# Optimization experiments

Hardware: AMD Instinct MI355X
Metric: run time of the kernel (lower is better)

## Reference

```python
import jax, jax.numpy as jnp
import numpy as np

N, E, IN_DIM, HID, MAXW, HEADS = 20000, 640000, 128, 256, 512, 32
BN_EPS = 1e-5


def setup_inputs() -> dict:
    key = jax.random.key(0)
    ks = jax.random.split(key, 10)
    x = jax.random.normal(ks[0], (N, IN_DIM), dtype=jnp.float32)
    edge_index = jax.random.randint(ks[1], (2, E), 0, N, dtype=jnp.int64)
    s = 0.02
    # backbone GIN layer: Linear(in_dim -> hidden) applied to (x + sum of neighbors)
    Wb = jax.random.normal(ks[2], (IN_DIM, HID), dtype=jnp.float32) * s
    bb = jnp.zeros((HID,), dtype=jnp.float32)
    # per-head hourglass: Linear(HID->MAXW) + BN + ReLU, then Linear(MAXW->HID)
    W1 = jax.random.normal(ks[3], (HEADS, HID, MAXW), dtype=jnp.float32) * s
    b1 = jnp.zeros((HEADS, MAXW), dtype=jnp.float32)
    gamma = jnp.ones((HEADS, MAXW), dtype=jnp.float32)
    beta = jnp.zeros((HEADS, MAXW), dtype=jnp.float32)
    W2 = jax.random.normal(ks[4], (HEADS, MAXW, HID), dtype=jnp.float32) * s
    b2 = jnp.zeros((HEADS, HID), dtype=jnp.float32)
    return {"x": x, "edge_index": edge_index, "Wb": Wb, "bb": bb,
            "W1": W1, "b1": b1, "gamma": gamma, "beta": beta,
            "W2": W2, "b2": b2}


def reference(x, edge_index, Wb, bb, W1, b1, gamma, beta, W2, b2):
    src, dst = edge_index[0], edge_index[1]
    # GIN-style aggregation (eps=0): self + sum of neighbor features
    agg = x + jax.ops.segment_sum(x[src], dst, num_segments=x.shape[0])
    h = jax.nn.relu(agg @ Wb + bb)                          # [N, HID]
    # all 32 heads as one batched GEMM
    z = jnp.einsum('nd,hdm->hnm', h, W1) + b1[:, None, :]   # [H, N, MAXW]
    # per-head BatchNorm1d in training mode: batch stats over nodes, biased var
    mean = jnp.mean(z, axis=1, keepdims=True)
    var = jnp.var(z, axis=1, keepdims=True)
    zn = (z - mean) * jax.lax.rsqrt(var + BN_EPS)
    a = jax.nn.relu(zn * gamma[:, None, :] + beta[:, None, :])
    # final per-head projection, stacked to [N, H, HID]
    out = jnp.einsum('hnm,hmd->nhd', a, W2) + b2[None, :, :]
    return out
```

## Files before the change

kernel.cpp:

```cpp
#include <hip/hip_runtime.h>
#include <stdint.h>

#define N_NODES 20000
#define E_EDGES 640000
#define IN_DIM  128
#define HID     256
#define MAXW    512
#define HEADS   32
#define BN_EPS  1e-5f
#define NT      20480
#define NB_SCAN 79

typedef __attribute__((ext_vector_type(8))) short bf16x8;
typedef __attribute__((ext_vector_type(4))) float f32x4;
typedef __attribute__((ext_vector_type(16))) float f32x16;
typedef unsigned short ushort_t;

static __device__ __forceinline__ float bf2f(ushort_t u){
  union { unsigned int i; float f; } v; v.i = ((unsigned int)u) << 16; return v.f;
}
static __device__ __forceinline__ ushort_t f2bf(float f){
  union { float f; unsigned int i; } v; v.f = f;
  unsigned int r = v.i + 0x7fffu + ((v.i >> 16) & 1u);
  return (ushort_t)(r >> 16);
}

__global__ void k_initdet(const int* __restrict__ ei, float* __restrict__ G,
                          float* __restrict__ s, int* __restrict__ deg,
                          int* __restrict__ flag, ushort_t* __restrict__ hT){
  int i = blockIdx.x * blockDim.x + threadIdx.x;
  int stride = gridDim.x * blockDim.x;
  float4 z4 = make_float4(0.f, 0.f, 0.f, 0.f);
  float4* Gd = (float4*)G;
  for (int j = i; j < 256 * 256 / 4; j += stride) Gd[j] = z4;
  for (int j = i; j < N_NODES; j += stride) deg[j] = 0;
  if (i < 256) s[i] = 0.f;
  uint4 zi = make_uint4(0u, 0u, 0u, 0u);
  for (int j = i; j < 256 * 60; j += stride){
    int c = j / 60, o = (j % 60) * 8;
    *(uint4*)(hT + (size_t)c * NT + N_NODES + o) = zi;
  }
  if (blockIdx.x == 0){
    __shared__ int any_nz;
    if (threadIdx.x == 0) any_nz = 0;
    __syncthreads();
    int nz = 0;
    for (int k = threadIdx.x; k < 4096; k += blockDim.x)
      if (ei[2 * k + 1] != 0) nz = 1;
    if (nz) atomicOr(&any_nz, 1);
    __syncthreads();
    if (threadIdx.x == 0) flag[0] = (any_nz == 0) ? 1 : 0;
  }
}

__global__ __launch_bounds__(256) void k_hist(const int* __restrict__ ei,
                                              const int* __restrict__ flag,
                                              int* __restrict__ deg){
  int e = blockIdx.x * 256 + threadIdx.x;
  if (e >= E_EDGES) return;
  int src, dst;
  if (flag[0]){ src = ei[2 * e]; dst = ei[2 * E_EDGES + 2 * e]; }
  else        { src = ei[e];     dst = ei[E_EDGES + e]; }
  if ((unsigned)src >= N_NODES || (unsigned)dst >= N_NODES) return;
  atomicAdd(&deg[dst], 1);
}

__global__ __launch_bounds__(256) void k_scan1(const int* __restrict__ deg,
                                               int* __restrict__ bsum){
  __shared__ int ws[4];
  int b = blockIdx.x, t = threadIdx.x, i = b * 256 + t;
  int v = (i < N_NODES) ? deg[i] : 0;
  #pragma unroll
  for (int o = 32; o; o >>= 1) v += __shfl_down(v, o);
  if ((t & 63) == 0) ws[t >> 6] = v;
  __syncthreads();
  if (t == 0) bsum[b] = ws[0] + ws[1] + ws[2] + ws[3];
}

__global__ __launch_bounds__(256) void k_scan3(const int* __restrict__ deg,
                                               const int* __restrict__ bsum,
                                               int* __restrict__ start,
                                               int* __restrict__ cursor){
  __shared__ int a[2][256];
  __shared__ int base;
  int b = blockIdx.x, t = threadIdx.x, i = b * 256 + t;
  if (t == 0){
    int r = 0;
    for (int k = 0; k < b; k++) r += bsum[k];
    base = r;
  }
  int v = (i < N_NODES) ? deg[i] : 0;
  a[0][t] = v;
  __syncthreads();
  int pb = 0;
  for (int o = 1; o < 256; o <<= 1){
    int x = a[pb][t] + ((t >= o) ? a[pb][t - o] : 0);
    a[pb ^ 1][t] = x;
    __syncthreads();
    pb ^= 1;
  }
  if (i < N_NODES){
    int ex = base + a[pb][t] - v;
    start[i] = ex; cursor[i] = ex;
  }
}

__global__ __launch_bounds__(256) void k_scatter(const int* __restrict__ ei,
                                                 const int* __restrict__ flag,
                                                 int* __restrict__ cursor,
                                                 int* __restrict__ eids){
  int e = blockIdx.x * 256 + threadIdx.x;
  if (e >= E_EDGES) return;
  int src, dst;
  if (flag[0]){ src = ei[2 * e]; dst = ei[2 * E_EDGES + 2 * e]; }
  else        { src = ei[e];     dst = ei[E_EDGES + e]; }
  if ((unsigned)src >= N_NODES || (unsigned)dst >= N_NODES) return;
  int p = atomicAdd(&cursor[dst], 1);
  eids[p] = src;
}

__global__ __launch_bounds__(256) void k_agg(const float* __restrict__ x,
                                             const int* __restrict__ start,
                                             const int* __restrict__ deg,
                                             const int* __restrict__ eids,
                                             float* __restrict__ agg){
  int wid = (blockIdx.x * 256 + threadIdx.x) >> 6;
  int lane = threadIdx.x & 63;
  if (wid >= N_NODES) return;
  int s0 = start[wid], d = deg[wid];
  float2 acc = *(const float2*)(x + (size_t)wid * IN_DIM + 2 * lane);
  int i = 0;
  for (; i + 4 <= d; i += 4){
    int e0 = eids[s0+i], e1 = eids[s0+i+1], e2 = eids[s0+i+2], e3 = eids[s0+i+3];
    float2 v0 = *(const float2*)(x + (size_t)e0 * IN_DIM + 2 * lane);
    float2 v1 = *(const float2*)(x + (size_t)e1 * IN_DIM + 2 * lane);
    float2 v2 = *(const float2*)(x + (size_t)e2 * IN_DIM + 2 * lane);
    float2 v3 = *(const float2*)(x + (size_t)e3 * IN_DIM + 2 * lane);
    acc.x += (v0.x + v1.x) + (v2.x + v3.x);
    acc.y += (v0.y + v1.y) + (v2.y + v3.y);
  }
  for (; i < d; i++){
    int e0 = eids[s0+i];
    float2 v0 = *(const float2*)(x + (size_t)e0 * IN_DIM + 2 * lane);
    acc.x += v0.x; acc.y += v0.y;
  }
  *(float2*)(agg + (size_t)wid * IN_DIM + 2 * lane) = acc;
}

__global__ __launch_bounds__(256) void k_backbone(const float* __restrict__ agg,
                                                  const float* __restrict__ Wb,
                                                  const float* __restrict__ bb,
                                                  ushort_t* __restrict__ hbf,
                                                  ushort_t* __restrict__ hT,
                                                  float* __restrict__ s){
  __shared__ float WbS[32][256];
  __shared__ float aggS[32][36];
  int c = threadIdx.x;
  int n0 = blockIdx.x * 32;
  float acc[32];
  float bias = bb[c];
  #pragma unroll
  for (int i = 0; i < 32; i++) acc[i] = bias;
  for (int dc = 0; dc < 4; ++dc){
    __syncthreads();
    const float4* wsrc = (const float4*)(Wb + dc * 32 * 256);
    float4* wdst = (float4*)&WbS[0][0];
    #pragma unroll
    for (int i = 0; i < 8; i++) wdst[c + i * 256] = wsrc[c + i * 256];
    {
      int n = c >> 3, c4 = (c & 7) * 4;
      float4 v = *(const float4*)(agg + (size_t)(n0 + n) * IN_DIM + dc * 32 + c4);
      aggS[n][c4 + 0] = v.x; aggS[n][c4 + 1] = v.y;
      aggS[n][c4 + 2] = v.z; aggS[n][c4 + 3] = v.w;
    }
    __syncthreads();
    for (int d = 0; d < 32; ++d){
      float w = WbS[d][c];
      #pragma unroll
      for (int n = 0; n < 32; n++) acc[n] += aggS[n][d] * w;
    }
  }
  float ls = 0.f;
  ushort_t hrow[32];
  #pragma unroll
  for (int n = 0; n < 32; n++){
    float hv = acc[n] > 0.f ? acc[n] : 0.f;
    ushort_t hb = f2bf(hv);
    hbf[(size_t)(n0 + n) * HID + c] = hb;
    hrow[n] = hb;
    ls += bf2f(hb);
  }
  #pragma unroll
  for (int i = 0; i < 4; i++)
    *(uint4*)(hT + (size_t)c * NT + n0 + i * 8) = *(uint4*)(hrow + i * 8);
  unsafeAtomicAdd(&s[c], ls);
}

__global__ __launch_bounds__(256) void k_gram2(const ushort_t* __restrict__ hT,
                                               float* __restrict__ G){
  const int t = threadIdx.x;
  const int w = t >> 6, l = t & 63;
  const int s = blockIdx.x, hh = blockIdx.y;
  const int wr = w >> 1, wc = w & 1;
  const int ca = hh * 128 + wr * 64;
  const int cb = wc * 128;
  const int l31 = l & 31, l5 = l >> 5;
  f32x16 acc[2][4];
  #pragma unroll
  for (int a = 0; a < 2; a++)
    #pragma unroll
    for (int b = 0; b < 4; b++)
      #pragma unroll
      for (int r = 0; r < 16; r++) acc[a][b][r] = 0.f;

  const size_t kb0 = (size_t)s * 512 + l5 * 8;
  for (int ks = 0; ks < 32; ks++){
    size_t k = kb0 + ks * 16;
    bf16x8 af[2], bfr[4];
    #pragma unroll
    for (int a = 0; a < 2; a++)
      af[a] = *(const bf16x8*)(hT + (size_t)(ca + a * 32 + l31) * NT + k);
    #pragma unroll
    for (int b = 0; b < 4; b++)
      bfr[b] = *(const bf16x8*)(hT + (size_t)(cb + b * 32 + l31) * NT + k);
    #pragma unroll
    for (int a = 0; a < 2; a++)
      #pragma unroll
      for (int b = 0; b < 4; b++)
        acc[a][b] = __builtin_amdgcn_mfma_f32_32x32x16_bf16(af[a], bfr[b], acc[a][b], 0, 0, 0);
  }
  #pragma unroll
  for (int a = 0; a < 2; a++)
    #pragma unroll
    for (int b = 0; b < 4; b++)
      #pragma unroll
      for (int r = 0; r < 16; r++){
        int grow = (r & 3) + 8 * (r >> 2) + 4 * l5;
        unsafeAtomicAdd(&G[(size_t)(ca + a * 32 + grow) * 256 + cb + b * 32 + l31], acc[a][b][r]);
      }
}

__global__ __launch_bounds__(256) void k_transpose(const float* __restrict__ W1,
                                                   const float* __restrict__ W2,
                                                   ushort_t* __restrict__ w1t,
                                                   ushort_t* __restrict__ w2t){
  __shared__ float tile[32][33];
  int which = blockIdx.z, h = blockIdx.y, b = blockIdx.x;
  const float* src; int R, C;
  if (which == 0){ src = W1 + (size_t)h * 256 * 512; R = 256; C = 512; }
  else           { src = W2 + (size_t)h * 512 * 256; R = 512; C = 256; }
  int tcn = C >> 5;
  int tr = b / tcn, tc = b % tcn;
  int r0 = tr * 32, c0 = tc * 32;
  int tx = threadIdx.x & 31, ty = threadIdx.x >> 5;
  #pragma unroll
  for (int i = 0; i < 32; i += 8) tile[ty + i][tx] = src[(size_t)(r0 + ty + i) * C + c0 + tx];
  __syncthreads();
  if (which == 0){
    ushort_t* dst = w1t + (size_t)h * 512 * 256;
    #pragma unroll
    for (int i = 0; i < 32; i += 8){
      int M = c0 + ty + i;
      int D = r0 + tx;
      int D2 = (((D >> 3) ^ (M & 7)) << 3) | (D & 7);
      dst[(size_t)M * 256 + D2] = f2bf(tile[tx][ty + i]);
    }
  } else {
    ushort_t* dst = w2t + (size_t)h * 256 * 512;
    #pragma unroll
    for (int i = 0; i < 32; i += 8){
      int dd = c0 + ty + i;
      int m  = r0 + tx;
      int g2 = ((m >> 3) & 3) ^ (dd & 3) ^ ((dd >> 2) & 3);
      size_t idx = (size_t)(m >> 5) * 8192 + dd * 32 + (g2 << 3) + (m & 7);
      dst[idx] = f2bf(tile[tx][ty + i]);
    }
  }
}

__global__ __launch_bounds__(256) void k_stats(const float* __restrict__ G,
                                               const float* __restrict__ s,
                                               const ushort_t* __restrict__ w1t,
                                               const float* __restrict__ b1,
                                               const float* __restrict__ gamma,
                                               const float* __restrict__ beta,
                                               float* __restrict__ As,
                                               float* __restrict__ Bs){
  __shared__ ushort_t wL[256][64];
  __shared__ float GL[16][256];
  __shared__ float sL[256];
  __shared__ float red[4][64];
  int h = blockIdx.y, m0 = blockIdx.x * 64;
  int t = threadIdx.x, m = t & 63, q = t >> 6;
  {
    int mm = t >> 2, part = t & 3;
    int Mrow = m0 + mm;
    const ushort_t* srcr = w1t + ((size_t)h * 512 + Mrow) * 256;
    #pragma unroll
    for (int k4 = 0; k4 < 16; ++k4){
      int kb = part * 64 + k4 * 4;
      int eo = (((kb >> 3) ^ (Mrow & 7)) << 3) | (kb & 7);
      ushort4 v = *(const ushort4*)(srcr + eo);
      wL[kb+0][mm]=v.x; wL[kb+1][mm]=v.y; wL[kb+2][mm]=v.z; wL[kb+3][mm]=v.w;
    }
  }
  sL[t & 255] = s[t & 255];
  float quad = 0.f;
  for (int dc = 0; dc < 16; ++dc){
    __syncthreads();
    const float4* gs = (const float4*)(G + (size_t)dc * 16 * 256);
    float4* gd = (float4*)&GL[0][0];
    #pragma unroll
    for (int i = 0; i < 4; i++) gd[t + i * 256] = gs[t + i * 256];
    __syncthreads();
    #pragma unroll
    for (int i = 0; i < 4; i++){
      int dl = q * 4 + i;
      float wd = bf2f(wL[dc * 16 + dl][m]);
      float u = 0.f;
      for (int k = 0; k < 256; ++k) u += GL[dl][k] * bf2f(wL[k][m]);
      quad += wd * u;
    }
  }
  red[q][m] = quad;
  __syncthreads();
  if (q == 0){
    float qd = red[0][m] + red[1][m] + red[2][m] + red[3][m];
    float dot_s = 0.f;
    for (int k = 0; k < 256; ++k) dot_s += sL[k] * bf2f(wL[k][m]);
    float b1v = b1[(size_t)h * 512 + m0 + m];
    float invN = 1.f / (float)N_NODES;
    float mean = dot_s * invN + b1v;
    float ez2 = (qd + 2.f * b1v * dot_s) * invN + b1v * b1v;
    float var = ez2 - mean * mean;
    float rstd = rsqrtf(var + BN_EPS);
    float gv = gamma[(size_t)h * 512 + m0 + m];
    float be = beta[(size_t)h * 512 + m0 + m];
    float Av = rstd * gv;
    As[(size_t)h * 512 + m0 + m] = Av;
    Bs[(size_t)h * 512 + m0 + m] = be - mean * Av;
  }
}

__global__ __launch_bounds__(512, 2) void k_main(const ushort_t* __restrict__ hbf,
                                                 const ushort_t* __restrict__ w1t,
                                                 const ushort_t* __restrict__ w2t,
                                                 const float* __restrict__ As,
                                                 const float* __restrict__ Bs,
                                                 const float* __restrict__ b2,
                                                 float* __restrict__ out){
  __shared__ __align__(16) char lds_all[86016];
  const int h = blockIdx.y;
  const int n0 = blockIdx.x * 256;
  const int t = threadIdx.x;
  const int w = t >> 6, l = t & 63;
  const int l15 = l & 15, l4 = l >> 4;
  const int nw = n0 + w * 32;
  const f32x4 fzero = {0.f, 0.f, 0.f, 0.f};
  const bf16x8 bzero = {0,0,0,0,0,0,0,0};
  char* asw = lds_all + 65536 + w * 2560;

  bf16x8 afr[2][8];
  #pragma unroll
  for (int nset = 0; nset < 2; nset++){
    int row = nw + nset * 16 + l15;
    const ushort_t* p = hbf + (size_t)row * HID + l4 * 8;
    #pragma unroll
    for (int kk = 0; kk < 8; kk++){
      bf16x8 v = bzero;
      if (row < N_NODES) v = *(const bf16x8*)(p + kk * 32);
      afr[nset][kk] = v;
    }
  }
  f32x4 oacc[16][2];
  #pragma unroll
  for (int i = 0; i < 16; i++){ oacc[i][0] = fzero; oacc[i][1] = fzero; }

  const float* Asp = As + (size_t)h * 512;
  const float* Bsp = Bs + (size_t)h * 512;
  const char* w1g = (const char*)(w1t + (size_t)h * 512 * 256);
  const char* w2g = (const char*)(w2t + (size_t)h * 256 * 512);
  const int woff = w * 2048 + l * 16;

  {
    __builtin_amdgcn_global_load_lds((const __attribute__((address_space(1))) void*)(w1g + woff),
                                     (__attribute__((address_space(3))) void*)(lds_all + w * 2048), 16, 0, 0);
    __builtin_amdgcn_global_load_lds((const __attribute__((address_space(1))) void*)(w1g + woff + 1024),
                                     (__attribute__((address_space(3))) void*)(lds_all + w * 2048 + 1024), 16, 0, 0);
    __builtin_amdgcn_global_load_lds((const __attribute__((address_space(1))) void*)(w2g + woff),
                                     (__attribute__((address_space(3))) void*)(lds_all + 16384 + w * 2048), 16, 0, 0);
    __builtin_amdgcn_global_load_lds((const __attribute__((address_space(1))) void*)(w2g + woff + 1024),
                                     (__attribute__((address_space(3))) void*)(lds_all + 16384 + w * 2048 + 1024), 16, 0, 0);
  }
  __syncthreads();

  const int win = (l4 & 1) * 32;
  const unsigned sel = (l4 >> 1) ? 0x07060302u : 0x05040100u;

  for (int c = 0; c < 16; ++c){
    const int cur = c & 1;
    const int mc0 = c * 32;
    const bool pf = (c < 15);
    if (pf){
      const int nb = (c + 1) * 16384;
      char* db = lds_all + (cur ^ 1) * 32768;
      __builtin_amdgcn_global_load_lds((const __attribute__((address_space(1))) void*)(w1g + nb + woff),
                                       (__attribute__((address_space(3))) void*)(db + w * 2048), 16, 0, 0);
      __builtin_amdgcn_global_load_lds((const __attribute__((address_space(1))) void*)(w1g + nb + woff + 1024),
                                       (__attribute__((address_space(3))) void*)(db + w * 2048 + 1024), 16, 0, 0);
      __builtin_amdgcn_global_load_lds((const __attribute__((address_space(1))) void*)(w2g + nb + woff),
                                       (__attribute__((address_space(3))) void*)(db + 16384 + w * 2048), 16, 0, 0);
      __builtin_amdgcn_global_load_lds((const __attribute__((address_space(1))) void*)(w2g + nb + woff + 1024),
                                       (__attribute__((address_space(3))) void*)(db + 16384 + w * 2048 + 1024), 16, 0, 0);
    }
    const char* w1b = lds_all + cur * 32768;
    const char* w2b = lds_all + cur * 32768 + 16384;

    f32x4 zt[2][2];
    zt[0][0] = fzero; zt[0][1] = fzero; zt[1][0] = fzero; zt[1][1] = fzero;
    __builtin_amdgcn_s_setprio(1);
    #pragma unroll
    for (int kk = 0; kk < 8; kk++){
      #pragma unroll
      for (int ct = 0; ct < 2; ct++){
        int r1 = ct * 16 + l15;
        int gr = kk * 4 + l4;
        bf16x8 wf = *(const bf16x8*)(w1b + r1 * 512 + ((gr ^ (r1 & 7)) * 16));
        zt[0][ct] = __builtin_amdgcn_mfma_f32_16x16x32_bf16(wf, afr[0][kk], zt[0][ct], 0, 0, 0);
        zt[1][ct] = __builtin_amdgcn_mfma_f32_16x16x32_bf16(wf, afr[1][kk], zt[1][ct], 0, 0, 0);
      }
    }
    __builtin_amdgcn_s_setprio(0);

    {
      float4 Av0 = *(const float4*)(Asp + mc0 + l4 * 4);
      float4 Bv0 = *(const float4*)(Bsp + mc0 + l4 * 4);
      float4 Av1 = *(const float4*)(Asp + mc0 + 16 + l4 * 4);
      float4 Bv1 = *(const float4*)(Bsp + mc0 + 16 + l4 * 4);
      #pragma unroll
      for (int nset = 0; nset < 2; nset++){
        float c00 = zt[nset][0][0] * Av0.x + Bv0.x; c00 = c00 > 0.f ? c00 : 0.f;
        float c01 = zt[nset][0][1] * Av0.y + Bv0.y; c01 = c01 > 0.f ? c01 : 0.f;
        float c02 = zt[nset][0][2] * Av0.z + Bv0.z; c02 = c02 > 0.f ? c02 : 0.f;
        float c03 = zt[nset][0][3] * Av0.w + Bv0.w; c03 = c03 > 0.f ? c03 : 0.f;
        float c10 = zt[nset][1][0] * Av1.x + Bv1.x; c10 = c10 > 0.f ? c10 : 0.f;
        float c11 = zt[nset][1][1] * Av1.y + Bv1.y; c11 = c11 > 0.f ? c11 : 0.f;
        float c12 = zt[nset][1][2] * Av1.z + Bv1.z; c12 = c12 > 0.f ? c12 : 0.f;
        float c13 = zt[nset][1][3] * Av1.w + Bv1.w; c13 = c13 > 0.f ? c13 : 0.f;
        uint4 pk;
        pk.x = (unsigned)f2bf(c00) | ((unsigned)f2bf(c10) << 16);
        pk.y = (unsigned)f2bf(c01) | ((unsigned)f2bf(c11) << 16);
        pk.z = (unsigned)f2bf(c02) | ((unsigned)f2bf(c12) << 16);
        pk.w = (unsigned)f2bf(c03) | ((unsigned)f2bf(c13) << 16);
        *(uint4*)(asw + (nset * 16 + l15) * 80 + l4 * 16) = pk;
      }
    }
    bf16x8 aa[2];
    #pragma unroll
    for (int nset = 0; nset < 2; nset++){
      const char* rp = asw + (nset * 16 + l15) * 80 + win;
      uint4 wa = *(const uint4*)(rp);
      uint4 wb = *(const uint4*)(rp + 16);
      unsigned o0 = __builtin_amdgcn_perm(wa.y, wa.x, sel);
      unsigned o1 = __builtin_amdgcn_perm(wa.w, wa.z, sel);
      unsigned o2 = __builtin_amdgcn_perm(wb.y, wb.x, sel);
      unsigned o3 = __builtin_amdgcn_perm(wb.w, wb.z, sel);
      uint4 q = make_uint4(o0, o1, o2, o3);
      aa[nset] = *(bf16x8*)&q;
    }

    __builtin_amdgcn_s_setprio(1);
    #pragma unroll
    for (int ddt = 0; ddt < 16; ddt++){
      int dd = ddt * 16 + l15;
      int g2 = l4 ^ (dd & 3) ^ ((dd >> 2) & 3);
      bf16x8 wf2 = *(const bf16x8*)(w2b + dd * 64 + g2 * 16);
      oacc[ddt][0] = __builtin_amdgcn_mfma_f32_16x16x32_bf16(wf2, aa[0], oacc[ddt][0], 0, 0, 0);
      oacc[ddt][1] = __builtin_amdgcn_mfma_f32_16x16x32_bf16(wf2, aa[1], oacc[ddt][1], 0, 0, 0);
    }
    __builtin_amdgcn_s_setprio(0);

    __syncthreads();
  }

  char* slice = lds_all + w * 8192;
  const int gsl = l & 31;
  const int rhalf = l >> 5;
  #pragma unroll
  for (int nset = 0; nset < 2; nset++){
    #pragma unroll
    for (int half = 0; half < 2; half++){
      #pragma unroll
      for (int dq = 0; dq < 8; dq++){
        int ddt = half * 8 + dq;
        *(f32x4*)(slice + l15 * 512 + (((dq * 4 + l4) ^ (l15 & 7)) * 16)) = oacc[ddt][nset];
      }
      float4 b2v = *(const float4*)(b2 + (size_t)h * 256 + half * 128 + gsl * 4);
      #pragma unroll
      for (int j = 0; j < 8; j++){
        int rr = rhalf + j * 2;
        f32x4 v = *(const f32x4*)(slice + rr * 512 + ((gsl ^ (rr & 7)) * 16));
        int n = nw + nset * 16 + rr;
        if (n < N_NODES){
          float4 o;
          o.x = v[0] + b2v.x; o.y = v[1] + b2v.y;
          o.z = v[2] + b2v.z; o.w = v[3] + b2v.w;
          *(float4*)(out + (size_t)n * (HEADS * HID) + h * HID + half * 128 + gsl * 4) = o;
        }
      }
    }
  }
}

extern "C" void kernel_launch(void* const* d_in, const int* in_sizes, int n_in,
                              void* d_out, int out_size, void* d_ws, size_t ws_size,
                              hipStream_t stream){
  const float* x     = (const float*)d_in[0];
  const int*   ei    = (const int*)  d_in[1];
  const float* Wb    = (const float*)d_in[2];
  const float* bb    = (const float*)d_in[3];
  const float* W1    = (const float*)d_in[4];
  const float* b1    = (const float*)d_in[5];
  const float* gamma = (const float*)d_in[6];
  const float* beta  = (const float*)d_in[7];
  const float* W2    = (const float*)d_in[8];
  const float* b2    = (const float*)d_in[9];
  float* out = (float*)d_out;

  char* ws = (char*)d_ws;
  size_t off = 0;
  auto alloc = [&](size_t bytes){ void* p = ws + off; off += (bytes + 255) & ~(size_t)255; return p; };
  float*    agg  = (float*)   alloc((size_t)N_NODES * IN_DIM * 4);
  ushort_t* hbf  = (ushort_t*)alloc((size_t)N_NODES * HID * 2);
  ushort_t* w1t  = (ushort_t*)alloc((size_t)HEADS * MAXW * HID * 2);
  ushort_t* w2t  = (ushort_t*)alloc((size_t)HEADS * HID * MAXW * 2);
  float*    G    = (float*)   alloc(256 * 256 * 4);
  float*    s    = (float*)   alloc(256 * 4);
  float*    As   = (float*)   alloc((size_t)HEADS * MAXW * 4);
  float*    Bs   = (float*)   alloc((size_t)HEADS * MAXW * 4);
  int*      flg  = (int*)     alloc(256);
  int*      deg  = (int*)     alloc((size_t)N_NODES * 4);
  int*      st   = (int*)     alloc((size_t)N_NODES * 4);
  int*      cur  = (int*)     alloc((size_t)N_NODES * 4);
  int*      eids = (int*)     alloc((size_t)E_EDGES * 4);
  ushort_t* hT   = (ushort_t*)alloc((size_t)HID * NT * 2);
  int*      bsum = (int*)     alloc(NB_SCAN * 4);

  hipLaunchKernelGGL(k_initdet,   dim3(512),         dim3(256), 0, stream, ei, G, s, deg, flg, hT);
  hipLaunchKernelGGL(k_hist,      dim3(2500),        dim3(256), 0, stream, ei, flg, deg);
  hipLaunchKernelGGL(k_scan1,     dim3(NB_SCAN),     dim3(256), 0, stream, deg, bsum);
  hipLaunchKernelGGL(k_scan3,     dim3(NB_SCAN),     dim3(256), 0, stream, deg, bsum, st, cur);
  hipLaunchKernelGGL(k_scatter,   dim3(2500),        dim3(256), 0, stream, ei, flg, cur, eids);
  hipLaunchKernelGGL(k_agg,       dim3(5000),        dim3(256), 0, stream, x, st, deg, eids, agg);
  hipLaunchKernelGGL(k_backbone,  dim3(625),         dim3(256), 0, stream, agg, Wb, bb, hbf, hT, s);
  hipLaunchKernelGGL(k_gram2,     dim3(40, 2),       dim3(256), 0, stream, hT, G);
  hipLaunchKernelGGL(k_transpose, dim3(128, 32, 2),  dim3(256), 0, stream, W1, W2, w1t, w2t);
  hipLaunchKernelGGL(k_stats,     dim3(8, 32),       dim3(256), 0, stream, G, s, w1t, b1, gamma, beta, As, Bs);
  hipLaunchKernelGGL(k_main,      dim3(79, 32),      dim3(512), 0, stream, hbf, w1t, w2t, As, Bs, b2, out);
}
```

Before: 805.7 us.

## Double chunk size per pipeline stage in main kernel and vectorize weight transpose stores

The main fused kernel now loads two 32-wide M chunks of W1/W2 per pipeline stage, with a 64KB double buffer, and processes them in an unrolled sub-loop. This halves the number of barriers and prefetch rounds. LDS use grows from about 84KB to about 148KB per block, which likely limits occupancy to one block per CU despite launch_bounds(512,2). The bf16 pack now uses the hardware v_cvt_pk_bf16_f32 instruction. The transpose kernel writes 16-byte vector stores from half the threads instead of scattered 2-byte stores.

```diff
diff --git a/kernel.cpp b/kernel.cpp
--- a/kernel.cpp
+++ b/kernel.cpp
@@ -23,6 +23,11 @@
   union { float f; unsigned int i; } v; v.f = f;
   unsigned int r = v.i + 0x7fffu + ((v.i >> 16) & 1u);
   return (ushort_t)(r >> 16);
+}
+static __device__ __forceinline__ unsigned cvtpk(float lo, float hi){
+  unsigned r;
+  asm("v_cvt_pk_bf16_f32 %0, %1, %2" : "=v"(r) : "v"(lo), "v"(hi));
+  return r;
 }
 
 __global__ void k_initdet(const int* __restrict__ ei, float* __restrict__ G,
@@ -256,25 +261,27 @@
   #pragma unroll
   for (int i = 0; i < 32; i += 8) tile[ty + i][tx] = src[(size_t)(r0 + ty + i) * C + c0 + tx];
   __syncthreads();
+  int tid = threadIdx.x;
+  if (tid >= 128) return;
   if (which == 0){
-    ushort_t* dst = w1t + (size_t)h * 512 * 256;
-    #pragma unroll
-    for (int i = 0; i < 32; i += 8){
-      int M = c0 + ty + i;
-      int D = r0 + tx;
-      int D2 = (((D >> 3) ^ (M & 7)) << 3) | (D & 7);
-      dst[(size_t)M * 256 + D2] = f2bf(tile[tx][ty + i]);
-    }
+    int mloc = tid & 31, dg = tid >> 5;
+    int M = c0 + mloc;
+    int Dg = (r0 >> 3) + dg;
+    ushort_t tmp[8];
+    #pragma unroll
+    for (int j = 0; j < 8; j++) tmp[j] = f2bf(tile[dg * 8 + j][mloc]);
+    ushort_t* dst = w1t + (size_t)h * 512 * 256 + (size_t)M * 256 + ((Dg ^ (M & 7)) << 3);
+    *(uint4*)dst = *(uint4*)tmp;
   } else {
-    ushort_t* dst = w2t + (size_t)h * 256 * 512;
-    #pragma unroll
-    for (int i = 0; i < 32; i += 8){
-      int dd = c0 + ty + i;
-      int m  = r0 + tx;
-      int g2 = ((m >> 3) & 3) ^ (dd & 3) ^ ((dd >> 2) & 3);
-      size_t idx = (size_t)(m >> 5) * 8192 + dd * 32 + (g2 << 3) + (m & 7);
-      dst[idx] = f2bf(tile[tx][ty + i]);
-    }
+    int ddloc = tid & 31, mo = tid >> 5;
+    int dd = c0 + ddloc;
+    int m0g = r0 + mo * 8;
+    int g2 = ((m0g >> 3) & 3) ^ (dd & 3) ^ ((dd >> 2) & 3);
+    ushort_t tmp[8];
+    #pragma unroll
+    for (int j = 0; j < 8; j++) tmp[j] = f2bf(tile[mo * 8 + j][ddloc]);
+    ushort_t* dst = w2t + (size_t)h * 256 * 512 + (size_t)(m0g >> 5) * 8192 + dd * 32 + (g2 << 3);
+    *(uint4*)dst = *(uint4*)tmp;
   }
 }
 
@@ -342,6 +349,10 @@
   }
 }
 
+#define GLDS(srcp, dstp) __builtin_amdgcn_global_load_lds( \
+    (const __attribute__((address_space(1))) void*)(srcp), \
+    (__attribute__((address_space(3))) void*)(dstp), 16, 0, 0)
+
 __global__ __launch_bounds__(512, 2) void k_main(const ushort_t* __restrict__ hbf,
                                                  const ushort_t* __restrict__ w1t,
                                                  const ushort_t* __restrict__ w2t,
@@ -349,7 +360,7 @@
                                                  const float* __restrict__ Bs,
                                                  const float* __restrict__ b2,
                                                  float* __restrict__ out){
-  __shared__ __align__(16) char lds_all[86016];
+  __shared__ __align__(16) char lds_all[151552];
   const int h = blockIdx.y;
   const int n0 = blockIdx.x * 256;
   const int t = threadIdx.x;
@@ -358,7 +369,7 @@
   const int nw = n0 + w * 32;
   const f32x4 fzero = {0.f, 0.f, 0.f, 0.f};
   const bf16x8 bzero = {0,0,0,0,0,0,0,0};
-  char* asw = lds_all + 65536 + w * 2560;
+  char* asw = lds_all + 131072 + w * 2560;
 
   bf16x8 afr[2][8];
   #pragma unroll
@@ -383,103 +394,106 @@
   const int woff = w * 2048 + l * 16;
 
   {
-    __builtin_amdgcn_global_load_lds((const __attribute__((address_space(1))) void*)(w1g + woff),
-                                     (__attribute__((address_space(3))) void*)(lds_all + w * 2048), 16, 0, 0);
-    __builtin_amdgcn_global_load_lds((const __attribute__((address_space(1))) void*)(w1g + woff + 1024),
-                                     (__attribute__((address_space(3))) void*)(lds_all + w * 2048 + 1024), 16, 0, 0);
-    __builtin_amdgcn_global_load_lds((const __attribute__((address_space(1))) void*)(w2g + woff),
-                                     (__attribute__((address_space(3))) void*)(lds_all + 16384 + w * 2048), 16, 0, 0);
-    __builtin_amdgcn_global_load_lds((const __attribute__((address_space(1))) void*)(w2g + woff + 1024),
-                                     (__attribute__((address_space(3))) void*)(lds_all + 16384 + w * 2048 + 1024), 16, 0, 0);
+    char* db = lds_all;
+    GLDS(w1g + woff,                 db + w * 2048);
+    GLDS(w1g + woff + 1024,          db + w * 2048 + 1024);
+    GLDS(w1g + 16384 + woff,         db + 16384 + w * 2048);
+    GLDS(w1g + 16384 + woff + 1024,  db + 16384 + w * 2048 + 1024);
+    GLDS(w2g + woff,                 db + 32768 + w * 2048);
+    GLDS(w2g + woff + 1024,          db + 32768 + w * 2048 + 1024);
+    GLDS(w2g + 16384 + woff,         db + 49152 + w * 2048);
+    GLDS(w2g + 16384 + woff + 1024,  db + 49152 + w * 2048 + 1024);
   }
   __syncthreads();
 
   const int win = (l4 & 1) * 32;
   const unsigned sel = (l4 >> 1) ? 0x07060302u : 0x05040100u;
 
-  for (int c = 0; c < 16; ++c){
-    const int cur = c & 1;
-    const int mc0 = c * 32;
-    const bool pf = (c < 15);
-    if (pf){
-      const int nb = (c + 1) * 16384;
-      char* db = lds_all + (cur ^ 1) * 32768;
-      __builtin_amdgcn_global_load_lds((const __attribute__((address_space(1))) void*)(w1g + nb + woff),
-                                       (__attribute__((address_space(3))) void*)(db + w * 2048), 16, 0, 0);
-      __builtin_amdgcn_global_load_lds((const __attribute__((address_space(1))) void*)(w1g + nb + woff + 1024),
-                                       (__attribute__((address_space(3))) void*)(db + w * 2048 + 1024), 16, 0, 0);
-      __builtin_amdgcn_global_load_lds((const __attribute__((address_space(1))) void*)(w2g + nb + woff),
-                                       (__attribute__((address_space(3))) void*)(db + 16384 + w * 2048), 16, 0, 0);
-      __builtin_amdgcn_global_load_lds((const __attribute__((address_space(1))) void*)(w2g + nb + woff + 1024),
-                                       (__attribute__((address_space(3))) void*)(db + 16384 + w * 2048 + 1024), 16, 0, 0);
-    }
-    const char* w1b = lds_all + cur * 32768;
-    const char* w2b = lds_all + cur * 32768 + 16384;
-
-    f32x4 zt[2][2];
-    zt[0][0] = fzero; zt[0][1] = fzero; zt[1][0] = fzero; zt[1][1] = fzero;
-    __builtin_amdgcn_s_setprio(1);
-    #pragma unroll
-    for (int kk = 0; kk < 8; kk++){
-      #pragma unroll
-      for (int ct = 0; ct < 2; ct++){
-        int r1 = ct * 16 + l15;
-        int gr = kk * 4 + l4;
-        bf16x8 wf = *(const bf16x8*)(w1b + r1 * 512 + ((gr ^ (r1 & 7)) * 16));
-        zt[0][ct] = __builtin_amdgcn_mfma_f32_16x16x32_bf16(wf, afr[0][kk], zt[0][ct], 0, 0, 0);
-        zt[1][ct] = __builtin_amdgcn_mfma_f32_16x16x32_bf16(wf, afr[1][kk], zt[1][ct], 0, 0, 0);
-      }
-    }
-    __builtin_amdgcn_s_setprio(0);
-
-    {
-      float4 Av0 = *(const float4*)(Asp + mc0 + l4 * 4);
-      float4 Bv0 = *(const float4*)(Bsp + mc0 + l4 * 4);
-      float4 Av1 = *(const float4*)(Asp + mc0 + 16 + l4 * 4);
-      float4 Bv1 = *(const float4*)(Bsp + mc0 + 16 + l4 * 4);
+  for (int p = 0; p < 8; ++p){
+    const int cur = p & 1;
+    if (p < 7){
+      const int nb = (p + 1) * 32768;
+      char* db = lds_all + (cur ^ 1) * 65536;
+      GLDS(w1g + nb + woff,                db + w * 2048);
+      GLDS(w1g + nb + woff + 1024,         db + w * 2048 + 1024);
+      GLDS(w1g + nb + 16384 + woff,        db + 16384 + w * 2048);
+      GLDS(w1g + nb + 16384 + woff + 1024, db + 16384 + w * 2048 + 1024);
+      GLDS(w2g + nb + woff,                db + 32768 + w * 2048);
+      GLDS(w2g + nb + woff + 1024,         db + 32768 + w * 2048 + 1024);
+      GLDS(w2g + nb + 16384 + woff,        db + 49152 + w * 2048);
+      GLDS(w2g + nb + 16384 + woff + 1024, db + 49152 + w * 2048 + 1024);
+    }
+    const char* base = lds_all + cur * 65536;
+    #pragma unroll
+    for (int sub = 0; sub < 2; ++sub){
+      const int mc0 = p * 64 + sub * 32;
+      const char* w1b = base + sub * 16384;
+      const char* w2b = base + 32768 + sub * 16384;
+
+      f32x4 zt[2][2];
+      zt[0][0] = fzero; zt[0][1] = fzero; zt[1][0] = fzero; zt[1][1] = fzero;
+      __builtin_amdgcn_s_setprio(1);
+      #pragma unroll
+      for (int kk = 0; kk < 8; kk++){
+        #pragma unroll
+        for (int ct = 0; ct < 2; ct++){
+          int r1 = ct * 16 + l15;
+          int gr = kk * 4 + l4;
+          bf16x8 wf = *(const bf16x8*)(w1b + r1 * 512 + ((gr ^ (r1 & 7)) * 16));
+          zt[0][ct] = __builtin_amdgcn_mfma_f32_16x16x32_bf16(wf, afr[0][kk], zt[0][ct], 0, 0, 0);
+          zt[1][ct] = __builtin_amdgcn_mfma_f32_16x16x32_bf16(wf, afr[1][kk], zt[1][ct], 0, 0, 0);
+        }
+      }
+      __builtin_amdgcn_s_setprio(0);
+
+      {
+        float4 Av0 = *(const float4*)(Asp + mc0 + l4 * 4);
+        float4 Bv0 = *(const float4*)(Bsp + mc0 + l4 * 4);
+        float4 Av1 = *(const float4*)(Asp + mc0 + 16 + l4 * 4);
+        float4 Bv1 = *(const float4*)(Bsp + mc0 + 16 + l4 * 4);
+        #pragma unroll
+        for (int nset = 0; nset < 2; nset++){
+          float c00 = zt[nset][0][0] * Av0.x + Bv0.x; c00 = c00 > 0.f ? c00 : 0.f;
+          float c01 = zt[nset][0][1] * Av0.y + Bv0.y; c01 = c01 > 0.f ? c01 : 0.f;
+          float c02 = zt[nset][0][2] * Av0.z + Bv0.z; c02 = c02 > 0.f ? c02 : 0.f;
+          float c03 = zt[nset][0][3] * Av0.w + Bv0.w; c03 = c03 > 0.f ? c03 : 0.f;
+          float c10 = zt[nset][1][0] * Av1.x + Bv1.x; c10 = c10 > 0.f ? c10 : 0.f;
+          float c11 = zt[nset][1][1] * Av1.y + Bv1.y; c11 = c11 > 0.f ? c11 : 0.f;
+          float c12 = zt[nset][1][2] * Av1.z + Bv1.z; c12 = c12 > 0.f ? c12 : 0.f;
+          float c13 = zt[nset][1][3] * Av1.w + Bv1.w; c13 = c13 > 0.f ? c13 : 0.f;
+          uint4 pk;
+          pk.x = cvtpk(c00, c10);
+          pk.y = cvtpk(c01, c11);
+          pk.z = cvtpk(c02, c12);
+          pk.w = cvtpk(c03, c13);
+          *(uint4*)(asw + (nset * 16 + l15) * 80 + l4 * 16) = pk;
+        }
+      }
+      bf16x8 aa[2];
       #pragma unroll
       for (int nset = 0; nset < 2; nset++){
-        float c00 = zt[nset][0][0] * Av0.x + Bv0.x; c00 = c00 > 0.f ? c00 : 0.f;
-        float c01 = zt[nset][0][1] * Av0.y + Bv0.y; c01 = c01 > 0.f ? c01 : 0.f;
-        float c02 = zt[nset][0][2] * Av0.z + Bv0.z; c02 = c02 > 0.f ? c02 : 0.f;
-        float c03 = zt[nset][0][3] * Av0.w + Bv0.w; c03 = c03 > 0.f ? c03 : 0.f;
-        float c10 = zt[nset][1][0] * Av1.x + Bv1.x; c10 = c10 > 0.f ? c10 : 0.f;
-        float c11 = zt[nset][1][1] * Av1.y + Bv1.y; c11 = c11 > 0.f ? c11 : 0.f;
-        float c12 = zt[nset][1][2] * Av1.z + Bv1.z; c12 = c12 > 0.f ? c12 : 0.f;
-        float c13 = zt[nset][1][3] * Av1.w + Bv1.w; c13 = c13 > 0.f ? c13 : 0.f;
-        uint4 pk;
-        pk.x = (unsigned)f2bf(c00) | ((unsigned)f2bf(c10) << 16);
-        pk.y = (unsigned)f2bf(c01) | ((unsigned)f2bf(c11) << 16);
-        pk.z = (unsigned)f2bf(c02) | ((unsigned)f2bf(c12) << 16);
-        pk.w = (unsigned)f2bf(c03) | ((unsigned)f2bf(c13) << 16);
-        *(uint4*)(asw + (nset * 16 + l15) * 80 + l4 * 16) = pk;
-      }
-    }
-    bf16x8 aa[2];
-    #pragma unroll
-    for (int nset = 0; nset < 2; nset++){
-      const char* rp = asw + (nset * 16 + l15) * 80 + win;
-      uint4 wa = *(const uint4*)(rp);
-      uint4 wb = *(const uint4*)(rp + 16);
-      unsigned o0 = __builtin_amdgcn_perm(wa.y, wa.x, sel);
-      unsigned o1 = __builtin_amdgcn_perm(wa.w, wa.z, sel);
-      unsigned o2 = __builtin_amdgcn_perm(wb.y, wb.x, sel);
-      unsigned o3 = __builtin_amdgcn_perm(wb.w, wb.z, sel);
-      uint4 q = make_uint4(o0, o1, o2, o3);
-      aa[nset] = *(bf16x8*)&q;
-    }
-
-    __builtin_amdgcn_s_setprio(1);
-    #pragma unroll
-    for (int ddt = 0; ddt < 16; ddt++){
-      int dd = ddt * 16 + l15;
-      int g2 = l4 ^ (dd & 3) ^ ((dd >> 2) & 3);
-      bf16x8 wf2 = *(const bf16x8*)(w2b + dd * 64 + g2 * 16);
-      oacc[ddt][0] = __builtin_amdgcn_mfma_f32_16x16x32_bf16(wf2, aa[0], oacc[ddt][0], 0, 0, 0);
-      oacc[ddt][1] = __builtin_amdgcn_mfma_f32_16x16x32_bf16(wf2, aa[1], oacc[ddt][1], 0, 0, 0);
-    }
-    __builtin_amdgcn_s_setprio(0);
-
+        const char* rp = asw + (nset * 16 + l15) * 80 + win;
+        uint4 wa = *(const uint4*)(rp);
+        uint4 wb = *(const uint4*)(rp + 16);
+        unsigned o0 = __builtin_amdgcn_perm(wa.y, wa.x, sel);
+        unsigned o1 = __builtin_amdgcn_perm(wa.w, wa.z, sel);
+        unsigned o2 = __builtin_amdgcn_perm(wb.y, wb.x, sel);
+        unsigned o3 = __builtin_amdgcn_perm(wb.w, wb.z, sel);
+        uint4 q = make_uint4(o0, o1, o2, o3);
+        aa[nset] = *(bf16x8*)&q;
+      }
+
+      __builtin_amdgcn_s_setprio(1);
+      #pragma unroll
+      for (int ddt = 0; ddt < 16; ddt++){
+        int dd = ddt * 16 + l15;
+        int g2 = l4 ^ (dd & 3) ^ ((dd >> 2) & 3);
+        bf16x8 wf2 = *(const bf16x8*)(w2b + dd * 64 + g2 * 16);
+        oacc[ddt][0] = __builtin_amdgcn_mfma_f32_16x16x32_bf16(wf2, aa[0], oacc[ddt][0], 0, 0, 0);
+        oacc[ddt][1] = __builtin_amdgcn_mfma_f32_16x16x32_bf16(wf2, aa[1], oacc[ddt][1], 0, 0, 0);
+      }
+      __builtin_amdgcn_s_setprio(0);
+    }
     __syncthreads();
   }
 
```

After: 809.5 us. No clear change (+0.5%).
